# Performance work log

Hardware: AMD Instinct MI355X
Metric: run time of the kernel (lower is better)

The kernel has to match this reference:

```python
import jax, jax.numpy as jnp
import numpy as np

T, B, A = 128, 512, 5
X, Y, Z, H, R = 2, 10, 32, 128, 128
LOG2PI = np.float32(np.log(2.0 * np.pi))


def setup_inputs() -> dict:
    key = jax.random.key(0)
    ks = iter(jax.random.split(key, 40))
    w = lambda *s: jax.random.normal(next(ks), s, jnp.float32) * 0.05
    return dict(
        states=jax.random.normal(next(ks), (T, B, Y), jnp.float32),
        eps=jax.random.normal(next(ks), (T - 1, B, A, Z), jnp.float32),
        enc_w1=w(A, X + Y + R, H), enc_b1=w(A, H),
        enc_w2=w(A, H, H), enc_b2=w(A, H),
        enc_mw=w(A, H, Z), enc_mb=w(A, Z),
        enc_sw=w(A, H, Z), enc_sb=w(A, Z),
        pri_w1=w(A, Y + R, H), pri_b1=w(A, H),
        pri_w2=w(A, H, H), pri_b2=w(A, H),
        pri_mw=w(A, H, Z), pri_mb=w(A, Z),
        pri_sw=w(A, H, Z), pri_sb=w(A, Z),
        dec_w1=w(A, Y + Z + R, H), dec_b1=w(A, H),
        dec_w2=w(A, H, H), dec_b2=w(A, H),
        dec_mw=w(A, H, X), dec_mb=w(A, X),
        dec_sw=w(A, H, X), dec_sb=w(A, X),
        gru_wih=w(A, X + Z, 3 * R), gru_whh=w(A, R, 3 * R),
        gru_bih=w(A, 3 * R), gru_bhh=w(A, 3 * R),
    )


def _lin(x, wt, b):
    # x: [B, A, I], wt: [A, I, O] -> [B, A, O]  (per-agent linear)
    return jnp.einsum('bai,aio->bao', x, wt) + b


def _mlp(x, w1, b1, w2, b2):
    return jax.nn.relu(_lin(jax.nn.relu(_lin(x, w1, b1)), w2, b2))


def reference(states, eps, enc_w1, enc_b1, enc_w2, enc_b2, enc_mw, enc_mb,
              enc_sw, enc_sb, pri_w1, pri_b1, pri_w2, pri_b2, pri_mw, pri_mb,
              pri_sw, pri_sb, dec_w1, dec_b1, dec_w2, dec_b2, dec_mw, dec_mb,
              dec_sw, dec_sb, gru_wih, gru_whh, gru_bih, gru_bhh):
    y_all = states[:-1]                              # [T-1, B, Y]
    x_all = states[1:].reshape(T - 1, B, A, X)       # per-agent next positions

    def step(carry, xs):
        h, kl, nll = carry                           # h: [B, A, R]
        y, x, e = xs                                 # y:[B,Y] x:[B,A,X] e:[B,A,Z]
        yb = jnp.broadcast_to(y[:, None, :], (B, A, Y))
        enc_h = _mlp(jnp.concatenate([x, yb, h], -1), enc_w1, enc_b1, enc_w2, enc_b2)
        enc_m = _lin(enc_h, enc_mw, enc_mb)
        enc_s = jax.nn.softplus(_lin(enc_h, enc_sw, enc_sb))
        pri_h = _mlp(jnp.concatenate([yb, h], -1), pri_w1, pri_b1, pri_w2, pri_b2)
        pri_m = _lin(pri_h, pri_mw, pri_mb)
        pri_s = jax.nn.softplus(_lin(pri_h, pri_sw, pri_sb))
        z = enc_m + enc_s * e                         # reparameterized sample
        dec_h = _mlp(jnp.concatenate([yb, z, h], -1), dec_w1, dec_b1, dec_w2, dec_b2)
        dec_m = _lin(dec_h, dec_mw, dec_mb)
        dec_s = jax.nn.softplus(_lin(dec_h, dec_sw, dec_sb))
        # GRU cell (torch gate order: r, z, n)
        gi = _lin(jnp.concatenate([x, z], -1), gru_wih, gru_bih)   # [B,A,3R]
        gh = _lin(h, gru_whh, gru_bhh)
        gir, giz, gin = jnp.split(gi, 3, -1)
        ghr, ghz, ghn = jnp.split(gh, 3, -1)
        r = jax.nn.sigmoid(gir + ghr)
        u = jax.nn.sigmoid(giz + ghz)
        n = jnp.tanh(gin + r * ghn)
        h_new = (1.0 - u) * n + u * h
        kl_t = 0.5 * jnp.sum(2.0 * jnp.log(pri_s) - 2.0 * jnp.log(enc_s)
                             + (enc_s ** 2 + (enc_m - pri_m) ** 2) / pri_s ** 2 - 1.0)
        nll_t = jnp.sum(0.5 * LOG2PI + jnp.log(dec_s) + 0.5 * ((x - dec_m) / dec_s) ** 2)
        return (h_new, kl + kl_t, nll + nll_t), None

    h0 = jnp.zeros((B, A, R), states.dtype)
    zero = jnp.zeros((), states.dtype)
    (h, kl, nll), _ = jax.lax.scan(step, (h0, zero, zero), (y_all, x_all, eps))
    return jnp.stack([kl, nll])  # [kl_loss, recon_loss]
```

## Files before the change

### kernel.cpp

```cpp
#include <hip/hip_runtime.h>

typedef __attribute__((ext_vector_type(8))) short bf16x8;
typedef __attribute__((ext_vector_type(4))) float f32x4;

#define MFMA_B16(A,B,C) __builtin_amdgcn_mfma_f32_16x16x32_bf16((A),(B),(C),0,0,0)

#define FO_ENC1 0
#define FO_PRI1 48
#define FO_DEC1 88
#define FO_GIH  136
#define FO_GHH  184
#define FO_ENC2 280
#define FO_PRI2 312
#define FO_DEC2 344
#define FO_MS   376
#define FO_DECMS 408
#define NFRAG   412

#define MS  200
#define TS  136

__device__ __forceinline__ unsigned short f2bf(float f) {
  union { float f; unsigned u; } v; v.f = f;
  unsigned r = (v.u + 0x7fffu + ((v.u >> 16) & 1u)) >> 16;
  return (unsigned short)r;
}
__device__ __forceinline__ float bf2f(unsigned short h) {
  union { unsigned u; float f; } v; v.u = ((unsigned)h) << 16;
  return v.f;
}
__device__ __forceinline__ float sigm_(float x) { return 1.f / (1.f + __expf(-x)); }
__device__ __forceinline__ float tanh_(float x) {
  x = fminf(fmaxf(x, -15.f), 15.f);
  float e = __expf(-2.f * x);
  return (1.f - e) / (1.f + e);
}
__device__ __forceinline__ float splus_(float x) {
  return fmaxf(x, 0.f) + log1pf(__expf(-fabsf(x)));
}
__device__ __forceinline__ void pin(bf16x8 &x) {
  f32x4 &r = reinterpret_cast<f32x4&>(x);
  asm volatile("" : "+v"(r));
}
__device__ __forceinline__ void pinf(float &x) { asm volatile("" : "+v"(x)); }

__global__ void prep_kernel(const float* __restrict__ ew1, const float* __restrict__ pw1,
                            const float* __restrict__ dw1, const float* __restrict__ wih,
                            const float* __restrict__ whh, const float* __restrict__ ew2,
                            const float* __restrict__ pw2, const float* __restrict__ dw2,
                            const float* __restrict__ emw, const float* __restrict__ esw,
                            const float* __restrict__ pmw, const float* __restrict__ psw,
                            const float* __restrict__ dmw, const float* __restrict__ dsw,
                            unsigned short* __restrict__ ws)
{
  int blk = blockIdx.x;
  int a = blk / NFRAG, f = blk % NFRAG;
  int l = threadIdx.x, lg = l >> 4, ln = l & 15;
  float v[8];

  if (f < FO_PRI1) {
    int fi = f, nt = fi / 6, kb = fi % 6, n = nt * 16 + ln;
#pragma unroll
    for (int j = 0; j < 8; ++j) {
      int mk = kb * 32 + lg * 8 + j;
      int r = (mk < 2) ? mk : (mk >= 34 && mk < 44) ? 2 + (mk - 34)
            : (mk >= 64) ? 12 + (mk - 64) : -1;
      v[j] = (r >= 0) ? ew1[((size_t)a * 140 + r) * 128 + n] : 0.f;
    }
  } else if (f < FO_DEC1) {
    int fi = f - FO_PRI1, nt = fi / 5, kb = 1 + fi % 5, n = nt * 16 + ln;
#pragma unroll
    for (int j = 0; j < 8; ++j) {
      int mk = kb * 32 + lg * 8 + j;
      int r = (mk >= 34 && mk < 44) ? (mk - 34) : (mk >= 64) ? 10 + (mk - 64) : -1;
      v[j] = (r >= 0) ? pw1[((size_t)a * 138 + r) * 128 + n] : 0.f;
    }
  } else if (f < FO_GIH) {
    int fi = f - FO_DEC1, nt = fi / 6, kb = fi % 6, n = nt * 16 + ln;
#pragma unroll
    for (int j = 0; j < 8; ++j) {
      int mk = kb * 32 + lg * 8 + j;
      int r = (mk >= 2 && mk < 34) ? 10 + (mk - 2) : (mk >= 34 && mk < 44) ? (mk - 34)
            : (mk >= 64) ? 42 + (mk - 64) : -1;
      v[j] = (r >= 0) ? dw1[((size_t)a * 170 + r) * 128 + n] : 0.f;
    }
  } else if (f < FO_GHH) {
    int fi = f - FO_GIH, nt = fi / 2, kb = fi % 2, n = nt * 16 + ln;
#pragma unroll
    for (int j = 0; j < 8; ++j) {
      int mk = kb * 32 + lg * 8 + j;
      v[j] = (mk < 34) ? wih[((size_t)a * 34 + mk) * 384 + n] : 0.f;
    }
  } else if (f < FO_ENC2) {
    int fi = f - FO_GHH, nt = fi / 4, kb = fi % 4, n = nt * 16 + ln;
#pragma unroll
    for (int j = 0; j < 8; ++j) {
      int r = kb * 32 + lg * 8 + j;
      v[j] = whh[((size_t)a * 128 + r) * 384 + n];
    }
  } else if (f < FO_DEC2) {
    int fi = f - FO_ENC2;
    const float* W = (fi < 32) ? ew2 : pw2;
    fi &= 31;
    int nt = fi / 4, kb = fi % 4, n = nt * 16 + ln;
#pragma unroll
    for (int j = 0; j < 8; ++j) {
      int r = kb * 32 + lg * 8 + j;
      v[j] = W[((size_t)a * 128 + r) * 128 + n];
    }
  } else if (f < FO_MS) {
    int fi = f - FO_DEC2, nt = fi / 4, kb = fi % 4, n = nt * 16 + ln;
#pragma unroll
    for (int j = 0; j < 8; ++j) {
      int r = kb * 32 + lg * 8 + j;
      v[j] = dw2[((size_t)a * 128 + r) * 128 + n];
    }
  } else if (f < FO_DECMS) {
    int fi = f - FO_MS, mat = fi / 8, rem = fi % 8, nt = rem / 4, kb = rem % 4;
    int n = nt * 16 + ln;
    const float* W = (mat == 0) ? emw : (mat == 1) ? esw : (mat == 2) ? pmw : psw;
#pragma unroll
    for (int j = 0; j < 8; ++j) {
      int r = kb * 32 + lg * 8 + j;
      v[j] = W[((size_t)a * 128 + r) * 32 + n];
    }
  } else {
    int kb = f - FO_DECMS;
#pragma unroll
    for (int j = 0; j < 8; ++j) {
      int r = kb * 32 + lg * 8 + j;
      v[j] = (ln < 2) ? dmw[((size_t)a * 128 + r) * 2 + ln]
           : (ln < 4) ? dsw[((size_t)a * 128 + r) * 2 + (ln - 2)] : 0.f;
    }
  }
  unsigned short* dst = ws + (size_t)blk * 512 + l * 8;
#pragma unroll
  for (int j = 0; j < 8; ++j) dst[j] = f2bf(v[j]);
}

__global__ __launch_bounds__(512, 1) void vrnn_main(
    const float* __restrict__ states, const float* __restrict__ eps,
    const float* __restrict__ eb1, const float* __restrict__ eb2,
    const float* __restrict__ emb, const float* __restrict__ esb,
    const float* __restrict__ pb1, const float* __restrict__ pb2,
    const float* __restrict__ pmb, const float* __restrict__ psb,
    const float* __restrict__ db1, const float* __restrict__ db2,
    const float* __restrict__ dmb, const float* __restrict__ dsb,
    const float* __restrict__ bih, const float* __restrict__ bhh,
    const unsigned short* __restrict__ frags, float* __restrict__ out)
{
  const int a = blockIdx.y;
  const int b0 = blockIdx.x * 16;
  const int tid = threadIdx.x;
  const int w = tid >> 6, l = tid & 63, lg = l >> 4, ln = l & 15;

  __shared__ __align__(16) unsigned short ghh_lds[96 * 512];
  __shared__ __align__(16) unsigned short ms_lds[32 * 512];
  __shared__ __align__(16) unsigned short dms_lds[4 * 512];
  __shared__ __align__(16) unsigned short master[16 * MS];
  __shared__ __align__(16) unsigned short t1e[16 * TS], t1p[16 * TS];
  __shared__ __align__(16) unsigned short he[16 * TS], hp[16 * TS];
  __shared__ float msbuf[2][16][32];
  __shared__ float red[16];

  const unsigned short* fa = frags + (size_t)a * NFRAG * 512;

  {
    const uint4* s1 = (const uint4*)(fa + (size_t)FO_GHH * 512);
    uint4* d1 = (uint4*)ghh_lds;
    for (int i = tid; i < 96 * 64; i += 512) d1[i] = s1[i];
    const uint4* s2 = (const uint4*)(fa + (size_t)FO_MS * 512);
    uint4* d2 = (uint4*)ms_lds;
    for (int i = tid; i < 32 * 64; i += 512) d2[i] = s2[i];
    const uint4* s3 = (const uint4*)(fa + (size_t)FO_DECMS * 512);
    uint4* d3 = (uint4*)dms_lds;
    if (tid < 256) d3[tid] = s3[tid];
  }
  for (int i = tid; i < 16 * MS; i += 512) master[i] = 0;

  bf16x8 be1[6], bp1[5], be2[4], bp2[4], bd2[4], bD[12];
#pragma unroll
  for (int kb = 0; kb < 6; ++kb) {
    be1[kb] = *(const bf16x8*)(fa + (size_t)(FO_ENC1 + w * 6 + kb) * 512 + l * 8);
    pin(be1[kb]);
  }
#pragma unroll
  for (int kb = 0; kb < 5; ++kb) {
    bp1[kb] = *(const bf16x8*)(fa + (size_t)(FO_PRI1 + w * 5 + kb) * 512 + l * 8);
    pin(bp1[kb]);
  }
#pragma unroll
  for (int kb = 0; kb < 4; ++kb) {
    be2[kb] = *(const bf16x8*)(fa + (size_t)(FO_ENC2 + w * 4 + kb) * 512 + l * 8);
    bp2[kb] = *(const bf16x8*)(fa + (size_t)(FO_PRI2 + w * 4 + kb) * 512 + l * 8);
    bd2[kb] = *(const bf16x8*)(fa + (size_t)(FO_DEC2 + w * 4 + kb) * 512 + l * 8);
    pin(be2[kb]); pin(bp2[kb]); pin(bd2[kb]);
  }
  if (w < 4) {
#pragma unroll
    for (int j = 0; j < 2; ++j)
#pragma unroll
      for (int kb = 0; kb < 6; ++kb)
        bD[j * 6 + kb] = *(const bf16x8*)(fa + (size_t)(FO_DEC1 + (w + 4 * j) * 6 + kb) * 512 + l * 8);
  } else {
    int kx = w - 4;
#pragma unroll
    for (int g = 0; g < 3; ++g)
#pragma unroll
      for (int j = 0; j < 2; ++j)
#pragma unroll
        for (int kb = 0; kb < 2; ++kb)
          bD[g * 4 + j * 2 + kb] =
            *(const bf16x8*)(fa + (size_t)(FO_GIH + (g * 8 + kx + 4 * j) * 2 + kb) * 512 + l * 8);
  }
#pragma unroll
  for (int i = 0; i < 12; ++i) pin(bD[i]);

  float eb1v = eb1[a * 128 + w * 16 + ln], pb1v = pb1[a * 128 + w * 16 + ln];
  float eb2v = eb2[a * 128 + w * 16 + ln], pb2v = pb2[a * 128 + w * 16 + ln];
  float db2v = db2[a * 128 + w * 16 + ln];
  float hbm = 0.f, hbs = 0.f, d1b0 = 0.f, d1b1 = 0.f, dmsb = 0.f;
  float ghb[6] = {0.f, 0.f, 0.f, 0.f, 0.f, 0.f};
  if (w < 2) { hbm = emb[a * 32 + w * 16 + ln]; hbs = esb[a * 32 + w * 16 + ln]; }
  else if (w < 4) { hbm = pmb[a * 32 + (w - 2) * 16 + ln]; hbs = psb[a * 32 + (w - 2) * 16 + ln]; }
  if (w < 4) { d1b0 = db1[a * 128 + w * 16 + ln]; d1b1 = db1[a * 128 + (w + 4) * 16 + ln]; }
  else {
    int kx = w - 4;
#pragma unroll
    for (int g = 0; g < 3; ++g)
#pragma unroll
      for (int j = 0; j < 2; ++j)
        ghb[g * 2 + j] = bih[a * 384 + g * 128 + (kx + 4 * j) * 16 + ln]
                       + bhh[a * 384 + g * 128 + (kx + 4 * j) * 16 + ln];
  }
  if (w == 0) dmsb = (ln < 2) ? dmb[a * 2 + ln] : (ln < 4) ? dsb[a * 2 + (ln - 2)] : 0.f;
  pinf(eb1v); pinf(pb1v); pinf(eb2v); pinf(pb2v); pinf(db2v);
  pinf(hbm); pinf(hbs); pinf(d1b0); pinf(d1b1); pinf(dmsb);
#pragma unroll
  for (int i = 0; i < 6; ++i) pinf(ghb[i]);

  __syncthreads();

  if (tid < 160) {
    int row = tid / 10, c = tid - row * 10;
    master[row * MS + 34 + c] = f2bf(states[(size_t)b0 * 10 + tid]);
  }
  if (tid >= 192 && tid < 224) {
    int i = tid - 192, row = i >> 1, c = i & 1;
    master[row * MS + c] = f2bf(states[((size_t)512 + b0 + row) * 10 + a * 2 + c]);
  }
  float e_cur[4] = {0.f, 0.f, 0.f, 0.f};
  if (w < 2) {
#pragma unroll
    for (int q = 0; q < 4; ++q)
      e_cur[q] = eps[((size_t)(b0 + 4 * lg + q) * 5 + a) * 32 + w * 16 + ln];
  }
  float xv[4] = {0.f, 0.f, 0.f, 0.f};
  float kl = 0.f, nll = 0.f;
  f32x4 em = {0, 0, 0, 0}, esv = {0, 0, 0, 0};
  f32x4 gh[3][2];
  float hn[8];
  __syncthreads();

  for (int t = 0; t < 127; ++t) {
    if (w == 0 && t > 0) {
      f32x4 acc = {dmsb, dmsb, dmsb, dmsb};
#pragma unroll
      for (int kb = 0; kb < 4; ++kb) {
        bf16x8 ad = *(const bf16x8*)&he[ln * TS + kb * 32 + lg * 8];
        bf16x8 bf = *(const bf16x8*)&dms_lds[kb * 512 + l * 8];
        acc = MFMA_B16(ad, bf, acc);
      }
#pragma unroll
      for (int q = 0; q < 4; ++q) {
        float sv = __shfl(splus_(acc[q]), l + 2);
        if (ln < 2) {
          float d = (xv[q] - acc[q]) / sv;
          nll += 0.9189385332f + __logf(sv) + 0.5f * d * d;
        }
      }
    }
    {
      bf16x8 am[6];
#pragma unroll
      for (int kb = 0; kb < 6; ++kb)
        am[kb] = *(const bf16x8*)&master[ln * MS + kb * 32 + lg * 8];
      f32x4 a1 = {eb1v, eb1v, eb1v, eb1v}, a2 = {pb1v, pb1v, pb1v, pb1v};
#pragma unroll
      for (int kb = 0; kb < 6; ++kb) a1 = MFMA_B16(am[kb], be1[kb], a1);
#pragma unroll
      for (int kb = 0; kb < 5; ++kb) a2 = MFMA_B16(am[kb + 1], bp1[kb], a2);
#pragma unroll
      for (int q = 0; q < 4; ++q) {
        t1e[(4 * lg + q) * TS + w * 16 + ln] = f2bf(fmaxf(a1[q], 0.f));
        t1p[(4 * lg + q) * TS + w * 16 + ln] = f2bf(fmaxf(a2[q], 0.f));
      }
    }
    __syncthreads();

    {
      bf16x8 ae[4], ap[4];
#pragma unroll
      for (int kb = 0; kb < 4; ++kb) {
        ae[kb] = *(const bf16x8*)&t1e[ln * TS + kb * 32 + lg * 8];
        ap[kb] = *(const bf16x8*)&t1p[ln * TS + kb * 32 + lg * 8];
      }
      f32x4 a1 = {eb2v, eb2v, eb2v, eb2v}, a2 = {pb2v, pb2v, pb2v, pb2v};
#pragma unroll
      for (int kb = 0; kb < 4; ++kb) {
        a1 = MFMA_B16(ae[kb], be2[kb], a1);
        a2 = MFMA_B16(ap[kb], bp2[kb], a2);
      }
#pragma unroll
      for (int q = 0; q < 4; ++q) {
        he[(4 * lg + q) * TS + w * 16 + ln] = f2bf(fmaxf(a1[q], 0.f));
        hp[(4 * lg + q) * TS + w * 16 + ln] = f2bf(fmaxf(a2[q], 0.f));
      }
    }
    __syncthreads();

    {
      float e_nxt[4] = {0.f, 0.f, 0.f, 0.f};
      if (w < 2 && t < 126) {
#pragma unroll
        for (int q = 0; q < 4; ++q)
          e_nxt[q] = eps[((size_t)((t + 1) * 512 + b0 + 4 * lg + q) * 5 + a) * 32 + w * 16 + ln];
      }
      if (w < 4) {
        const unsigned short* hsrc = (w < 2) ? he : hp;
        bf16x8 ah[4];
#pragma unroll
        for (int kb = 0; kb < 4; ++kb)
          ah[kb] = *(const bf16x8*)&hsrc[ln * TS + kb * 32 + lg * 8];
        int mbase = ((w < 2) ? 0 : 16) + (w & 1) * 4;
        f32x4 m = {hbm, hbm, hbm, hbm}, s = {hbs, hbs, hbs, hbs};
#pragma unroll
        for (int kb = 0; kb < 4; ++kb) {
          m = MFMA_B16(ah[kb], *(const bf16x8*)&ms_lds[(mbase + kb) * 512 + l * 8], m);
          s = MFMA_B16(ah[kb], *(const bf16x8*)&ms_lds[(mbase + 8 + kb) * 512 + l * 8], s);
        }
        if (w < 2) {
          em = m;
#pragma unroll
          for (int q = 0; q < 4; ++q) {
            esv[q] = splus_(s[q]);
            master[(4 * lg + q) * MS + 2 + w * 16 + ln] = f2bf(m[q] + esv[q] * e_cur[q]);
          }
        } else {
#pragma unroll
          for (int q = 0; q < 4; ++q) {
            msbuf[0][4 * lg + q][(w - 2) * 16 + ln] = m[q];
            msbuf[1][4 * lg + q][(w - 2) * 16 + ln] = splus_(s[q]);
          }
        }
      } else {
        int kx = w - 4;
        bf16x8 ahh[4];
#pragma unroll
        for (int kb = 0; kb < 4; ++kb)
          ahh[kb] = *(const bf16x8*)&master[ln * MS + (kb + 2) * 32 + lg * 8];
#pragma unroll
        for (int g = 0; g < 3; ++g)
#pragma unroll
          for (int j = 0; j < 2; ++j) {
            float bv = ghb[g * 2 + j];
            gh[g][j] = (f32x4){bv, bv, bv, bv};
          }
#pragma unroll
        for (int kb = 0; kb < 4; ++kb)
#pragma unroll
          for (int g = 0; g < 3; ++g)
#pragma unroll
            for (int j = 0; j < 2; ++j)
              gh[g][j] = MFMA_B16(ahh[kb],
                *(const bf16x8*)&ghh_lds[(size_t)((g * 8 + kx + 4 * j) * 4 + kb) * 512 + l * 8],
                gh[g][j]);
      }
      if (w < 2 && t < 126) {
#pragma unroll
        for (int q = 0; q < 4; ++q) e_cur[q] = e_nxt[q];
      }
    }
    __syncthreads();

    if (w == 0) {
#pragma unroll
      for (int q = 0; q < 4; ++q)
        xv[q] = states[((size_t)(t + 1) * 512 + b0 + 4 * lg + q) * 10 + a * 2 + (ln & 1)];
    }
    if (w < 4) {
      bf16x8 amn[6];
#pragma unroll
      for (int kb = 0; kb < 6; ++kb)
        amn[kb] = *(const bf16x8*)&master[ln * MS + kb * 32 + lg * 8];
#pragma unroll
      for (int j = 0; j < 2; ++j) {
        float bv = (j == 0) ? d1b0 : d1b1;
        f32x4 acc = {bv, bv, bv, bv};
#pragma unroll
        for (int kb = 0; kb < 6; ++kb) acc = MFMA_B16(amn[kb], bD[j * 6 + kb], acc);
#pragma unroll
        for (int q = 0; q < 4; ++q)
          t1e[(4 * lg + q) * TS + (w + 4 * j) * 16 + ln] = f2bf(fmaxf(acc[q], 0.f));
      }
      if (w < 2) {
#pragma unroll
        for (int q = 0; q < 4; ++q) {
          float pm = msbuf[0][4 * lg + q][w * 16 + ln];
          float ps = msbuf[1][4 * lg + q][w * 16 + ln];
          float dm = em[q] - pm;
          float es2 = esv[q] * esv[q];
          kl += 0.5f * (2.f * __logf(ps) - 2.f * __logf(esv[q]) + (es2 + dm * dm) / (ps * ps) - 1.f);
        }
      }
    } else {
      int kx = w - 4;
      bf16x8 am2[2];
#pragma unroll
      for (int kb = 0; kb < 2; ++kb)
        am2[kb] = *(const bf16x8*)&master[ln * MS + kb * 32 + lg * 8];
      f32x4 gi[3][2];
#pragma unroll
      for (int g = 0; g < 3; ++g)
#pragma unroll
        for (int j = 0; j < 2; ++j) gi[g][j] = (f32x4){0.f, 0.f, 0.f, 0.f};
#pragma unroll
      for (int kb = 0; kb < 2; ++kb)
#pragma unroll
        for (int g = 0; g < 3; ++g)
#pragma unroll
          for (int j = 0; j < 2; ++j)
            gi[g][j] = MFMA_B16(am2[kb], bD[g * 4 + j * 2 + kb], gi[g][j]);
#pragma unroll
      for (int j = 0; j < 2; ++j)
#pragma unroll
        for (int q = 0; q < 4; ++q) {
          float r_ = sigm_(gi[0][j][q] + gh[0][j][q]);
          float u_ = sigm_(gi[1][j][q] + gh[1][j][q]);
          float n_ = tanh_(gi[2][j][q] + r_ * gh[2][j][q]);
          float ho = bf2f(master[(4 * lg + q) * MS + 64 + (kx + 4 * j) * 16 + ln]);
          hn[j * 4 + q] = (1.f - u_) * n_ + u_ * ho;
        }
    }
    __syncthreads();

    {
      bf16x8 ad[4];
#pragma unroll
      for (int kb = 0; kb < 4; ++kb)
        ad[kb] = *(const bf16x8*)&t1e[ln * TS + kb * 32 + lg * 8];
      f32x4 acc = {db2v, db2v, db2v, db2v};
#pragma unroll
      for (int kb = 0; kb < 4; ++kb) acc = MFMA_B16(ad[kb], bd2[kb], acc);
#pragma unroll
      for (int q = 0; q < 4; ++q)
        he[(4 * lg + q) * TS + w * 16 + ln] = f2bf(fmaxf(acc[q], 0.f));
    }
    if (w >= 4) {
      int kx = w - 4;
#pragma unroll
      for (int j = 0; j < 2; ++j)
#pragma unroll
        for (int q = 0; q < 4; ++q)
          master[(4 * lg + q) * MS + 64 + (kx + 4 * j) * 16 + ln] = f2bf(hn[j * 4 + q]);
    }
    if (t < 126) {
      if (w >= 1 && w <= 3) {
        int i = (w - 1) * 64 + l;
        if (i < 160) {
          int row = i / 10, c = i - row * 10;
          master[row * MS + 34 + c] = f2bf(states[((size_t)(t + 1) * 512 + b0) * 10 + i]);
        }
      }
      if (w == 0 && l < 32) {
        int row = l >> 1, c = l & 1;
        master[row * MS + c] = f2bf(states[((size_t)(t + 2) * 512 + b0 + row) * 10 + a * 2 + c]);
      }
    }
    __syncthreads();
  }

  if (w == 0) {
    f32x4 acc = {dmsb, dmsb, dmsb, dmsb};
#pragma unroll
    for (int kb = 0; kb < 4; ++kb) {
      bf16x8 ad = *(const bf16x8*)&he[ln * TS + kb * 32 + lg * 8];
      bf16x8 bf = *(const bf16x8*)&dms_lds[kb * 512 + l * 8];
      acc = MFMA_B16(ad, bf, acc);
    }
#pragma unroll
    for (int q = 0; q < 4; ++q) {
      float sv = __shfl(splus_(acc[q]), l + 2);
      if (ln < 2) {
        float d = (xv[q] - acc[q]) / sv;
        nll += 0.9189385332f + __logf(sv) + 0.5f * d * d;
      }
    }
  }

#pragma unroll
  for (int off = 32; off > 0; off >>= 1) {
    kl += __shfl_down(kl, off);
    nll += __shfl_down(nll, off);
  }
  if (l == 0) { red[w] = kl; red[8 + w] = nll; }
  __syncthreads();
  if (tid == 0) {
    float K = 0.f, N = 0.f;
#pragma unroll
    for (int i = 0; i < 8; ++i) { K += red[i]; N += red[8 + i]; }
    atomicAdd(out, K);
    atomicAdd(out + 1, N);
  }
}

extern "C" void kernel_launch(void* const* d_in, const int* in_sizes, int n_in,
                              void* d_out, int out_size, void* d_ws, size_t ws_size,
                              hipStream_t stream) {
  (void)in_sizes; (void)n_in; (void)out_size; (void)ws_size;
  const float* states = (const float*)d_in[0];
  const float* eps    = (const float*)d_in[1];
  const float* ew1 = (const float*)d_in[2];
  const float* eb1 = (const float*)d_in[3];
  const float* ew2 = (const float*)d_in[4];
  const float* eb2 = (const float*)d_in[5];
  const float* emw = (const float*)d_in[6];
  const float* emb = (const float*)d_in[7];
  const float* esw = (const float*)d_in[8];
  const float* esb = (const float*)d_in[9];
  const float* pw1 = (const float*)d_in[10];
  const float* pb1 = (const float*)d_in[11];
  const float* pw2 = (const float*)d_in[12];
  const float* pb2 = (const float*)d_in[13];
  const float* pmw = (const float*)d_in[14];
  const float* pmb = (const float*)d_in[15];
  const float* psw = (const float*)d_in[16];
  const float* psb = (const float*)d_in[17];
  const float* dw1 = (const float*)d_in[18];
  const float* db1 = (const float*)d_in[19];
  const float* dw2 = (const float*)d_in[20];
  const float* db2 = (const float*)d_in[21];
  const float* dmw = (const float*)d_in[22];
  const float* dmb = (const float*)d_in[23];
  const float* dsw = (const float*)d_in[24];
  const float* dsb = (const float*)d_in[25];
  const float* wih = (const float*)d_in[26];
  const float* whh = (const float*)d_in[27];
  const float* bih = (const float*)d_in[28];
  const float* bhh = (const float*)d_in[29];

  unsigned short* frags = (unsigned short*)d_ws;
  float* out = (float*)d_out;

  hipMemsetAsync(d_out, 0, 2 * sizeof(float), stream);
  prep_kernel<<<dim3(5 * NFRAG), dim3(64), 0, stream>>>(
      ew1, pw1, dw1, wih, whh, ew2, pw2, dw2, emw, esw, pmw, psw, dmw, dsw, frags);
  vrnn_main<<<dim3(32, 5), dim3(512), 0, stream>>>(
      states, eps, eb1, eb2, emb, esb, pb1, pb2, pmb, psb,
      db1, db2, dmb, dsb, bih, bhh, frags, out);
}
```

Before: 1.090 ms.

## Stream weight fragments from global per step and rebalance GRU work across all waves

Stops keeping the bf16 weight fragments in registers and the GRU hidden-weight matrix in LDS, and instead reloads them from global (L2-cached) memory inside every timestep. The launch bound moves from 1 to 2 blocks per CU, so two blocks can share a CU and hide each other's latency. The GRU hidden and input gate matmuls are spread across all 8 waves, and the decoder layer-1 work is split the same way, instead of the old 4/4 wave specialisation. The cost is many more global loads inside the serial recurrence, which adds load latency on the critical path of every step.

Result: slower. 1.629 ms (+49.5%).

```diff
diff --git a/kernel.cpp b/kernel.cpp
--- a/kernel.cpp
+++ b/kernel.cpp
@@ -38,11 +38,6 @@
 __device__ __forceinline__ float splus_(float x) {
   return fmaxf(x, 0.f) + log1pf(__expf(-fabsf(x)));
 }
-__device__ __forceinline__ void pin(bf16x8 &x) {
-  f32x4 &r = reinterpret_cast<f32x4&>(x);
-  asm volatile("" : "+v"(r));
-}
-__device__ __forceinline__ void pinf(float &x) { asm volatile("" : "+v"(x)); }
 
 __global__ void prep_kernel(const float* __restrict__ ew1, const float* __restrict__ pw1,
                             const float* __restrict__ dw1, const float* __restrict__ wih,
@@ -138,7 +133,9 @@
   for (int j = 0; j < 8; ++j) dst[j] = f2bf(v[j]);
 }
 
-__global__ __launch_bounds__(512, 1) void vrnn_main(
+#define LD_FRAG(idx) (*(const bf16x8*)(fa + (size_t)(idx) * 512 + l * 8))
+
+__global__ __launch_bounds__(512, 2) void vrnn_main(
     const float* __restrict__ states, const float* __restrict__ eps,
     const float* __restrict__ eb1, const float* __restrict__ eb2,
     const float* __restrict__ emb, const float* __restrict__ esb,
@@ -154,7 +151,6 @@
   const int tid = threadIdx.x;
   const int w = tid >> 6, l = tid & 63, lg = l >> 4, ln = l & 15;
 
-  __shared__ __align__(16) unsigned short ghh_lds[96 * 512];
   __shared__ __align__(16) unsigned short ms_lds[32 * 512];
   __shared__ __align__(16) unsigned short dms_lds[4 * 512];
   __shared__ __align__(16) unsigned short master[16 * MS];
@@ -166,9 +162,6 @@
   const unsigned short* fa = frags + (size_t)a * NFRAG * 512;
 
   {
-    const uint4* s1 = (const uint4*)(fa + (size_t)FO_GHH * 512);
-    uint4* d1 = (uint4*)ghh_lds;
-    for (int i = tid; i < 96 * 64; i += 512) d1[i] = s1[i];
     const uint4* s2 = (const uint4*)(fa + (size_t)FO_MS * 512);
     uint4* d2 = (uint4*)ms_lds;
     for (int i = tid; i < 32 * 64; i += 512) d2[i] = s2[i];
@@ -178,66 +171,18 @@
   }
   for (int i = tid; i < 16 * MS; i += 512) master[i] = 0;
 
-  bf16x8 be1[6], bp1[5], be2[4], bp2[4], bd2[4], bD[12];
-#pragma unroll
-  for (int kb = 0; kb < 6; ++kb) {
-    be1[kb] = *(const bf16x8*)(fa + (size_t)(FO_ENC1 + w * 6 + kb) * 512 + l * 8);
-    pin(be1[kb]);
-  }
-#pragma unroll
-  for (int kb = 0; kb < 5; ++kb) {
-    bp1[kb] = *(const bf16x8*)(fa + (size_t)(FO_PRI1 + w * 5 + kb) * 512 + l * 8);
-    pin(bp1[kb]);
-  }
-#pragma unroll
-  for (int kb = 0; kb < 4; ++kb) {
-    be2[kb] = *(const bf16x8*)(fa + (size_t)(FO_ENC2 + w * 4 + kb) * 512 + l * 8);
-    bp2[kb] = *(const bf16x8*)(fa + (size_t)(FO_PRI2 + w * 4 + kb) * 512 + l * 8);
-    bd2[kb] = *(const bf16x8*)(fa + (size_t)(FO_DEC2 + w * 4 + kb) * 512 + l * 8);
-    pin(be2[kb]); pin(bp2[kb]); pin(bd2[kb]);
-  }
-  if (w < 4) {
-#pragma unroll
-    for (int j = 0; j < 2; ++j)
-#pragma unroll
-      for (int kb = 0; kb < 6; ++kb)
-        bD[j * 6 + kb] = *(const bf16x8*)(fa + (size_t)(FO_DEC1 + (w + 4 * j) * 6 + kb) * 512 + l * 8);
-  } else {
-    int kx = w - 4;
-#pragma unroll
-    for (int g = 0; g < 3; ++g)
-#pragma unroll
-      for (int j = 0; j < 2; ++j)
-#pragma unroll
-        for (int kb = 0; kb < 2; ++kb)
-          bD[g * 4 + j * 2 + kb] =
-            *(const bf16x8*)(fa + (size_t)(FO_GIH + (g * 8 + kx + 4 * j) * 2 + kb) * 512 + l * 8);
-  }
-#pragma unroll
-  for (int i = 0; i < 12; ++i) pin(bD[i]);
-
   float eb1v = eb1[a * 128 + w * 16 + ln], pb1v = pb1[a * 128 + w * 16 + ln];
   float eb2v = eb2[a * 128 + w * 16 + ln], pb2v = pb2[a * 128 + w * 16 + ln];
   float db2v = db2[a * 128 + w * 16 + ln];
-  float hbm = 0.f, hbs = 0.f, d1b0 = 0.f, d1b1 = 0.f, dmsb = 0.f;
-  float ghb[6] = {0.f, 0.f, 0.f, 0.f, 0.f, 0.f};
+  float d1b  = db1[a * 128 + w * 16 + ln];
+  float ghb[3];
+#pragma unroll
+  for (int g = 0; g < 3; ++g)
+    ghb[g] = bih[a * 384 + g * 128 + w * 16 + ln] + bhh[a * 384 + g * 128 + w * 16 + ln];
+  float hbm = 0.f, hbs = 0.f, dmsb = 0.f;
   if (w < 2) { hbm = emb[a * 32 + w * 16 + ln]; hbs = esb[a * 32 + w * 16 + ln]; }
   else if (w < 4) { hbm = pmb[a * 32 + (w - 2) * 16 + ln]; hbs = psb[a * 32 + (w - 2) * 16 + ln]; }
-  if (w < 4) { d1b0 = db1[a * 128 + w * 16 + ln]; d1b1 = db1[a * 128 + (w + 4) * 16 + ln]; }
-  else {
-    int kx = w - 4;
-#pragma unroll
-    for (int g = 0; g < 3; ++g)
-#pragma unroll
-      for (int j = 0; j < 2; ++j)
-        ghb[g * 2 + j] = bih[a * 384 + g * 128 + (kx + 4 * j) * 16 + ln]
-                       + bhh[a * 384 + g * 128 + (kx + 4 * j) * 16 + ln];
-  }
   if (w == 0) dmsb = (ln < 2) ? dmb[a * 2 + ln] : (ln < 4) ? dsb[a * 2 + (ln - 2)] : 0.f;
-  pinf(eb1v); pinf(pb1v); pinf(eb2v); pinf(pb2v); pinf(db2v);
-  pinf(hbm); pinf(hbs); pinf(d1b0); pinf(d1b1); pinf(dmsb);
-#pragma unroll
-  for (int i = 0; i < 6; ++i) pinf(ghb[i]);
 
   __syncthreads();
 
@@ -258,8 +203,8 @@
   float xv[4] = {0.f, 0.f, 0.f, 0.f};
   float kl = 0.f, nll = 0.f;
   f32x4 em = {0, 0, 0, 0}, esv = {0, 0, 0, 0};
-  f32x4 gh[3][2];
-  float hn[8];
+  f32x4 gh[3];
+  float hn[4];
   __syncthreads();
 
   for (int t = 0; t < 127; ++t) {
@@ -281,15 +226,20 @@
       }
     }
     {
+      bf16x8 f1[6], f2[5];
+#pragma unroll
+      for (int kb = 0; kb < 6; ++kb) f1[kb] = LD_FRAG(FO_ENC1 + w * 6 + kb);
+#pragma unroll
+      for (int kb = 0; kb < 5; ++kb) f2[kb] = LD_FRAG(FO_PRI1 + w * 5 + kb);
       bf16x8 am[6];
 #pragma unroll
       for (int kb = 0; kb < 6; ++kb)
         am[kb] = *(const bf16x8*)&master[ln * MS + kb * 32 + lg * 8];
       f32x4 a1 = {eb1v, eb1v, eb1v, eb1v}, a2 = {pb1v, pb1v, pb1v, pb1v};
 #pragma unroll
-      for (int kb = 0; kb < 6; ++kb) a1 = MFMA_B16(am[kb], be1[kb], a1);
-#pragma unroll
-      for (int kb = 0; kb < 5; ++kb) a2 = MFMA_B16(am[kb + 1], bp1[kb], a2);
+      for (int kb = 0; kb < 6; ++kb) a1 = MFMA_B16(am[kb], f1[kb], a1);
+#pragma unroll
+      for (int kb = 0; kb < 5; ++kb) a2 = MFMA_B16(am[kb + 1], f2[kb], a2);
 #pragma unroll
       for (int q = 0; q < 4; ++q) {
         t1e[(4 * lg + q) * TS + w * 16 + ln] = f2bf(fmaxf(a1[q], 0.f));
@@ -299,6 +249,12 @@
     __syncthreads();
 
     {
+      bf16x8 f1[4], f2[4];
+#pragma unroll
+      for (int kb = 0; kb < 4; ++kb) {
+        f1[kb] = LD_FRAG(FO_ENC2 + w * 4 + kb);
+        f2[kb] = LD_FRAG(FO_PRI2 + w * 4 + kb);
+      }
       bf16x8 ae[4], ap[4];
 #pragma unroll
       for (int kb = 0; kb < 4; ++kb) {
@@ -308,13 +264,30 @@
       f32x4 a1 = {eb2v, eb2v, eb2v, eb2v}, a2 = {pb2v, pb2v, pb2v, pb2v};
 #pragma unroll
       for (int kb = 0; kb < 4; ++kb) {
-        a1 = MFMA_B16(ae[kb], be2[kb], a1);
-        a2 = MFMA_B16(ap[kb], bp2[kb], a2);
+        a1 = MFMA_B16(ae[kb], f1[kb], a1);
+        a2 = MFMA_B16(ap[kb], f2[kb], a2);
       }
 #pragma unroll
       for (int q = 0; q < 4; ++q) {
         he[(4 * lg + q) * TS + w * 16 + ln] = f2bf(fmaxf(a1[q], 0.f));
         hp[(4 * lg + q) * TS + w * 16 + ln] = f2bf(fmaxf(a2[q], 0.f));
+      }
+    }
+    {
+      bf16x8 ahh[4];
+#pragma unroll
+      for (int kb = 0; kb < 4; ++kb)
+        ahh[kb] = *(const bf16x8*)&master[ln * MS + (kb + 2) * 32 + lg * 8];
+#pragma unroll
+      for (int g = 0; g < 3; ++g) {
+        bf16x8 fg[4];
+#pragma unroll
+        for (int kb = 0; kb < 4; ++kb)
+          fg[kb] = LD_FRAG(FO_GHH + (g * 8 + w) * 4 + kb);
+        float bv = ghb[g];
+        gh[g] = (f32x4){bv, bv, bv, bv};
+#pragma unroll
+        for (int kb = 0; kb < 4; ++kb) gh[g] = MFMA_B16(ahh[kb], fg[kb], gh[g]);
       }
     }
     __syncthreads();
@@ -353,28 +326,6 @@
             msbuf[1][4 * lg + q][(w - 2) * 16 + ln] = splus_(s[q]);
           }
         }
-      } else {
-        int kx = w - 4;
-        bf16x8 ahh[4];
-#pragma unroll
-        for (int kb = 0; kb < 4; ++kb)
-          ahh[kb] = *(const bf16x8*)&master[ln * MS + (kb + 2) * 32 + lg * 8];
-#pragma unroll
-        for (int g = 0; g < 3; ++g)
-#pragma unroll
-          for (int j = 0; j < 2; ++j) {
-            float bv = ghb[g * 2 + j];
-            gh[g][j] = (f32x4){bv, bv, bv, bv};
-          }
-#pragma unroll
-        for (int kb = 0; kb < 4; ++kb)
-#pragma unroll
-          for (int g = 0; g < 3; ++g)
-#pragma unroll
-            for (int j = 0; j < 2; ++j)
-              gh[g][j] = MFMA_B16(ahh[kb],
-                *(const bf16x8*)&ghh_lds[(size_t)((g * 8 + kx + 4 * j) * 4 + kb) * 512 + l * 8],
-                gh[g][j]);
       }
       if (w < 2 && t < 126) {
 #pragma unroll
@@ -383,25 +334,44 @@
     }
     __syncthreads();
 
-    if (w == 0) {
+    {
+      if (w == 0) {
+#pragma unroll
+        for (int q = 0; q < 4; ++q)
+          xv[q] = states[((size_t)(t + 1) * 512 + b0 + 4 * lg + q) * 10 + a * 2 + (ln & 1)];
+      }
+      bf16x8 fd[6];
+#pragma unroll
+      for (int kb = 0; kb < 6; ++kb) fd[kb] = LD_FRAG(FO_DEC1 + w * 6 + kb);
+      bf16x8 am[6];
+#pragma unroll
+      for (int kb = 0; kb < 6; ++kb)
+        am[kb] = *(const bf16x8*)&master[ln * MS + kb * 32 + lg * 8];
+      f32x4 acc = {d1b, d1b, d1b, d1b};
+#pragma unroll
+      for (int kb = 0; kb < 6; ++kb) acc = MFMA_B16(am[kb], fd[kb], acc);
 #pragma unroll
       for (int q = 0; q < 4; ++q)
-        xv[q] = states[((size_t)(t + 1) * 512 + b0 + 4 * lg + q) * 10 + a * 2 + (ln & 1)];
-    }
-    if (w < 4) {
-      bf16x8 amn[6];
-#pragma unroll
-      for (int kb = 0; kb < 6; ++kb)
-        amn[kb] = *(const bf16x8*)&master[ln * MS + kb * 32 + lg * 8];
-#pragma unroll
-      for (int j = 0; j < 2; ++j) {
-        float bv = (j == 0) ? d1b0 : d1b1;
-        f32x4 acc = {bv, bv, bv, bv};
-#pragma unroll
-        for (int kb = 0; kb < 6; ++kb) acc = MFMA_B16(amn[kb], bD[j * 6 + kb], acc);
-#pragma unroll
-        for (int q = 0; q < 4; ++q)
-          t1e[(4 * lg + q) * TS + (w + 4 * j) * 16 + ln] = f2bf(fmaxf(acc[q], 0.f));
+        t1e[(4 * lg + q) * TS + w * 16 + ln] = f2bf(fmaxf(acc[q], 0.f));
+
+      f32x4 gi[3];
+#pragma unroll
+      for (int g = 0; g < 3; ++g) {
+        bf16x8 fg[2];
+#pragma unroll
+        for (int kb = 0; kb < 2; ++kb)
+          fg[kb] = LD_FRAG(FO_GIH + (g * 8 + w) * 2 + kb);
+        gi[g] = (f32x4){0.f, 0.f, 0.f, 0.f};
+#pragma unroll
+        for (int kb = 0; kb < 2; ++kb) gi[g] = MFMA_B16(am[kb], fg[kb], gi[g]);
+      }
+#pragma unroll
+      for (int q = 0; q < 4; ++q) {
+        float r_ = sigm_(gi[0][q] + gh[0][q]);
+        float u_ = sigm_(gi[1][q] + gh[1][q]);
+        float n_ = tanh_(gi[2][q] + r_ * gh[2][q]);
+        float ho = bf2f(master[(4 * lg + q) * MS + 64 + w * 16 + ln]);
+        hn[q] = (1.f - u_) * n_ + u_ * ho;
       }
       if (w < 2) {
 #pragma unroll
@@ -413,57 +383,27 @@
           kl += 0.5f * (2.f * __logf(ps) - 2.f * __logf(esv[q]) + (es2 + dm * dm) / (ps * ps) - 1.f);
         }
       }
-    } else {
-      int kx = w - 4;
-      bf16x8 am2[2];
-#pragma unroll
-      for (int kb = 0; kb < 2; ++kb)
-        am2[kb] = *(const bf16x8*)&master[ln * MS + kb * 32 + lg * 8];
-      f32x4 gi[3][2];
-#pragma unroll
-      for (int g = 0; g < 3; ++g)
-#pragma unroll
-        for (int j = 0; j < 2; ++j) gi[g][j] = (f32x4){0.f, 0.f, 0.f, 0.f};
-#pragma unroll
-      for (int kb = 0; kb < 2; ++kb)
-#pragma unroll
-        for (int g = 0; g < 3; ++g)
-#pragma unroll
-          for (int j = 0; j < 2; ++j)
-            gi[g][j] = MFMA_B16(am2[kb], bD[g * 4 + j * 2 + kb], gi[g][j]);
-#pragma unroll
-      for (int j = 0; j < 2; ++j)
-#pragma unroll
-        for (int q = 0; q < 4; ++q) {
-          float r_ = sigm_(gi[0][j][q] + gh[0][j][q]);
-          float u_ = sigm_(gi[1][j][q] + gh[1][j][q]);
-          float n_ = tanh_(gi[2][j][q] + r_ * gh[2][j][q]);
-          float ho = bf2f(master[(4 * lg + q) * MS + 64 + (kx + 4 * j) * 16 + ln]);
-          hn[j * 4 + q] = (1.f - u_) * n_ + u_ * ho;
-        }
     }
     __syncthreads();
 
     {
+      bf16x8 fd2[4];
+#pragma unroll
+      for (int kb = 0; kb < 4; ++kb) fd2[kb] = LD_FRAG(FO_DEC2 + w * 4 + kb);
       bf16x8 ad[4];
 #pragma unroll
       for (int kb = 0; kb < 4; ++kb)
         ad[kb] = *(const bf16x8*)&t1e[ln * TS + kb * 32 + lg * 8];
       f32x4 acc = {db2v, db2v, db2v, db2v};
 #pragma unroll
-      for (int kb = 0; kb < 4; ++kb) acc = MFMA_B16(ad[kb], bd2[kb], acc);
+      for (int kb = 0; kb < 4; ++kb) acc = MFMA_B16(ad[kb], fd2[kb], acc);
 #pragma unroll
       for (int q = 0; q < 4; ++q)
         he[(4 * lg + q) * TS + w * 16 + ln] = f2bf(fmaxf(acc[q], 0.f));
     }
-    if (w >= 4) {
-      int kx = w - 4;
-#pragma unroll
-      for (int j = 0; j < 2; ++j)
-#pragma unroll
-        for (int q = 0; q < 4; ++q)
-          master[(4 * lg + q) * MS + 64 + (kx + 4 * j) * 16 + ln] = f2bf(hn[j * 4 + q]);
-    }
+#pragma unroll
+    for (int q = 0; q < 4; ++q)
+      master[(4 * lg + q) * MS + 64 + w * 16 + ln] = f2bf(hn[q]);
     if (t < 126) {
       if (w >= 1 && w <= 3) {
         int i = (w - 1) * 64 + l;
```
